# Kernel tuning notes

Hardware: AMD Instinct MI355X
Metric: run time of the kernel (lower is better)

The kernel has to match this reference:

```python
import jax, jax.numpy as jnp
import numpy as np

# ---- geometry constants (from init_kwargs options) ----
VIEWS, NDET, NX, NY = 360, 736, 512, 512
DVOX, DDET = 0.7, 1.2858
DSO, DOD = 595.0, 490.6
DSD = DSO + DOD
STEP = 0.0174533
END_ANGLE = STEP * VIEWS  # ~2*pi
EXTENT = 1


def _compute_indices():
    """CPU port of PixelIndexCal_cuda (fanflat mode, extent=1).
    Returns flat int64 indices of shape [NX*NY*VIEWS] (pixel-major, view inner)."""
    sVx, sVy = DVOX * NX, DVOX * NY
    alphas = np.linspace(0.0, END_ANGLE, VIEWS, endpoint=False)
    indX, indY = np.meshgrid(np.arange(NX, dtype=np.float64),
                             np.arange(NY, dtype=np.float64), indexing='ij')
    idx_all = np.empty((NX * NY, VIEWS), dtype=np.int64)
    for a in range(VIEWS):
        alpha = -alphas[a]
        c, s = np.cos(alpha), np.sin(alpha)
        P0x = -(sVx / 2 - DVOX / 2)
        P0y = sVy / 2 - DVOX / 2
        rot = lambda px, py: (px * c + py * s, -px * s + py * c)
        Px_, Py_ = rot(P0x, P0y)
        Pxx, Pxy = rot(P0x + DVOX, P0y)
        Pyx, Pyy = rot(P0x, P0y - DVOX)
        Py_, Pxy, Pyy = Py_ / DDET, Pxy / DDET, Pyy / DDET
        dXx, dXy = Pxx - Px_, Pxy - Py_
        dYx, dYy = Pyx - Px_, Pyy - Py_
        # per-pixel rotated coords
        Pix = Px_ + indX * dXx + indY * dYx
        Piy = Py_ + indX * dXy + indY * dYy
        # fanflat: source at (DSO, 0); ray hits detector plane at x = DSO-DSD
        vectX = Pix - DSO
        t = -DSD / vectX
        det = Piy * t + NDET / 2.0
        det = np.clip(det, 1.0, NDET - 2.0)
        idx_all[:, a] = (det + NDET * a).astype(np.int64).ravel()
    return idx_all.reshape(-1)


def _conv(x, w, b):
    y = jax.lax.conv_general_dilated(x, w, (1, 1), 'SAME',
                                     dimension_numbers=('NCHW', 'OIHW', 'NCHW'))
    return y + b[None, :, None, None]


def setup_inputs() -> dict:
    key = jax.random.key(0)
    ks = jax.random.split(key, 16)
    lin_std = 1.0 / np.sqrt(NDET)
    conv_std = 1.0 / np.sqrt(64 * 9)
    inp = {
        'x': jax.random.normal(ks[0], (1, 1, VIEWS, NDET), jnp.float32),
        'indices': jnp.asarray(_compute_indices()),
        'w1': jax.random.normal(ks[1], (NDET, NDET), jnp.float32) * lin_std,
        'b1': jnp.zeros((NDET,), jnp.float32),
        'w2': jax.random.normal(ks[2], (NDET, NDET), jnp.float32) * lin_std,
        'b2': jnp.zeros((NDET,), jnp.float32),
        'conv_in_w': jax.random.normal(ks[3], (64, 1, 3, 3), jnp.float32) * (1.0 / 3.0),
        'conv_in_b': jnp.zeros((64,), jnp.float32),
        'blk_w1': jax.random.normal(ks[4], (11, 64, 64, 3, 3), jnp.float32) * conv_std,
        'blk_b1': jnp.zeros((11, 64), jnp.float32),
        'blk_w2': jax.random.normal(ks[5], (11, 64, 64, 3, 3), jnp.float32) * conv_std,
        'blk_b2': jnp.zeros((11, 64), jnp.float32),
        'conv_out_w': jax.random.normal(ks[6], (1, 64, 3, 3), jnp.float32) * conv_std,
        'conv_out_b': jnp.zeros((1,), jnp.float32),
    }
    return inp


def reference(x, indices, w1, b1, w2, b2, conv_in_w, conv_in_b,
              blk_w1, blk_b1, blk_w2, blk_b2, conv_out_w, conv_out_b):
    # convf: two per-detector-row Linear+ReLU over last dim (nDetecU)
    h = jax.nn.relu(x @ w1.T + b1)
    h = jax.nn.relu(h @ w2.T + b2)
    # BackProjNet (learn=False): gather + sum over views, scale, flip
    sino = h.reshape(-1, 1, VIEWS * NDET)
    g = sino[:, :, indices]                         # [B,1,NX*NY*VIEWS]
    g = g.reshape(-1, 1, NX * NY, VIEWS * EXTENT)
    img = g.sum(axis=3) * ((END_ANGLE - 0.0) / (2 * VIEWS * EXTENT))
    img = img.reshape(-1, 1, NX, NY)
    img = jnp.flip(img, axis=(2, 3))
    # rCNN refinement: conv(1->64)+ReLU, 11 residual blocks, conv(64->1)
    y = jax.nn.relu(_conv(img, conv_in_w, conv_in_b))
    for i in range(11):
        z = _conv(y, blk_w1[i], blk_b1[i])
        z = jax.nn.relu(z)
        z = _conv(z, blk_w2[i], blk_b2[i])
        y = jax.nn.relu(y + z)
    out = _conv(y, conv_out_w, conv_out_b)
    return out
```

## Files before the change

### kernel.cpp

```cpp
#include <hip/hip_runtime.h>

#define VIEWS 360
#define NDET 736
#define NX 512
#define NY 512
#define NPIX (NX * NY)

typedef unsigned short u16;
typedef __attribute__((ext_vector_type(8))) short bf16x8;
typedef __attribute__((ext_vector_type(4))) float f32x4;

__device__ __forceinline__ u16 f2bf(float f) {
  unsigned u = __float_as_uint(f);
  return (u16)((u + 0x7fffu + ((u >> 16) & 1u)) >> 16);
}

__global__ __launch_bounds__(256) void linear_relu_kernel(
    const float* __restrict__ in, const float* __restrict__ w,
    const float* __restrict__ b, float* __restrict__ out) {
  __shared__ __align__(16) float xin[NDET];
  const int v = blockIdx.x;
  const float4* src4 = (const float4*)(in + v * NDET);
  float4* dst4 = (float4*)xin;
  for (int k = threadIdx.x; k < NDET / 4; k += 256) dst4[k] = src4[k];
  __syncthreads();

  for (int d = threadIdx.x; d < NDET; d += 256) {
    const float4* w4 = (const float4*)(w + d * NDET);
    float acc = 0.f;
#pragma unroll 8
    for (int k = 0; k < NDET / 4; ++k) {
      float4 xv = ((const float4*)xin)[k];
      float4 wv = w4[k];
      acc = fmaf(xv.x, wv.x, acc);
      acc = fmaf(xv.y, wv.y, acc);
      acc = fmaf(xv.z, wv.z, acc);
      acc = fmaf(xv.w, wv.w, acc);
    }
    out[v * NDET + d] = fmaxf(acc + b[d], 0.f);
  }
}

__global__ __launch_bounds__(256) void backproj_kernel(
    const float* __restrict__ sino, const int* __restrict__ idx,
    float* __restrict__ img) {
  __shared__ int lidx[256 * 77];
  const int t = threadIdx.x;
  const int p_base = blockIdx.x * 256;

  float a0 = 0.f, a1 = 0.f, a2 = 0.f, a3 = 0.f;

#pragma unroll 1
  for (int c = 0; c < 5; ++c) {
    if (c) __syncthreads();
#pragma unroll
    for (int k = 0; k < 18; ++k) {
      const int f = k * 256 + t;
      const int row = f / 18, col4 = f % 18;
      int4 v = *(const int4*)&idx[(size_t)(p_base + row) * VIEWS + c * 72 +
                                  col4 * 4];
      int* dst = &lidx[row * 77 + col4 * 4];
      dst[0] = v.x; dst[1] = v.y; dst[2] = v.z; dst[3] = v.w;
    }
    __syncthreads();
    const int* myrow = &lidx[t * 77];
#pragma unroll
    for (int j = 0; j < 72; j += 4) {
      a0 += sino[myrow[j + 0]];
      a1 += sino[myrow[j + 1]];
      a2 += sino[myrow[j + 2]];
      a3 += sino[myrow[j + 3]];
    }
  }

  const int p = p_base + t;
  const int ix = p >> 9, iy = p & 511;
  img[(NX - 1 - ix) * NY + (NY - 1 - iy)] =
      ((a0 + a1) + (a2 + a3)) * 0.00872665f;
}

__device__ __forceinline__ void load9(const float* __restrict__ base, int gx,
                                      int gy, float v[9]) {
  const bool xm = gx > 0, xp = gx < NX - 1, ym = gy > 0, yp = gy < NY - 1;
  const float* c = base + gy * NX + gx;
  v[0] = (ym && xm) ? c[-NX - 1] : 0.f;
  v[1] = (ym)       ? c[-NX]     : 0.f;
  v[2] = (ym && xp) ? c[-NX + 1] : 0.f;
  v[3] = (xm)       ? c[-1]      : 0.f;
  v[4] =               c[0];
  v[5] = (xp)       ? c[1]       : 0.f;
  v[6] = (yp && xm) ? c[NX - 1]  : 0.f;
  v[7] = (yp)       ? c[NX]      : 0.f;
  v[8] = (yp && xp) ? c[NX + 1]  : 0.f;
}

__device__ __forceinline__ float dot9(float a, const float v[9],
                                      const float* __restrict__ w) {
  a = fmaf(v[0], w[0], a);
  a = fmaf(v[1], w[1], a);
  a = fmaf(v[2], w[2], a);
  a = fmaf(v[3], w[3], a);
  a = fmaf(v[4], w[4], a);
  a = fmaf(v[5], w[5], a);
  a = fmaf(v[6], w[6], a);
  a = fmaf(v[7], w[7], a);
  a = fmaf(v[8], w[8], a);
  return a;
}

__global__ __launch_bounds__(256) void conv_in_kernel(
    const float* __restrict__ in, const float* __restrict__ w,
    const float* __restrict__ b, float* __restrict__ out) {
  const int p = blockIdx.x * 256 + threadIdx.x;
  const int gx = p & (NX - 1), gy = p >> 9;
  float v[9];
  load9(in, gx, gy, v);
  float4* o = (float4*)(out + (size_t)p * 64);
#pragma unroll
  for (int oq = 0; oq < 16; ++oq) {
    float4 r;
    r.x = fmaxf(dot9(b[oq * 4 + 0], v, w + (oq * 4 + 0) * 9), 0.f);
    r.y = fmaxf(dot9(b[oq * 4 + 1], v, w + (oq * 4 + 1) * 9), 0.f);
    r.z = fmaxf(dot9(b[oq * 4 + 2], v, w + (oq * 4 + 2) * 9), 0.f);
    r.w = fmaxf(dot9(b[oq * 4 + 3], v, w + (oq * 4 + 3) * 9), 0.f);
    o[oq] = r;
  }
}

__global__ __launch_bounds__(256) void prep_weights_kernel(
    const float* __restrict__ bw1, const float* __restrict__ bw2,
    u16* __restrict__ wR) {
  const int g = blockIdx.x * 256 + threadIdx.x;
  if (g >= 22 * 36864) return;
  const int li = g / 36864, r1 = g % 36864;
  const int s = r1 / 2048, r2 = r1 % 2048;
  const int lane = r2 / 32, r3 = r2 % 32;
  const int mf = r3 / 8, j = r3 % 8;
  const int tap = s >> 1, kb = s & 1;
  const int kg = lane >> 4, n = lane & 15;
  const int oc = mf * 16 + n;
  const int ic = kb * 32 + kg * 8 + j;
  const float* src = (li < 11) ? bw1 + li * 36864 : bw2 + (li - 11) * 36864;
  wR[g] = f2bf(src[(oc * 64 + ic) * 9 + tap]);
}

template <int IN_BF, int OUT_BF, int RELU, int ADDRES>
__global__ __launch_bounds__(256, 3) void conv64_mfma(
    const void* __restrict__ in_, const u16* __restrict__ wA,
    const float* __restrict__ bias, const float* __restrict__ res,
    void* __restrict__ out_) {
  __shared__ u16 lds[6 * 66 * 64];
  const int xb = (blockIdx.x & 7) * 64;
  const int yb = (int)(blockIdx.x >> 3) * 4;
  const int tid = threadIdx.x;

#pragma unroll 1
  for (int it = 0; it < 13; ++it) {
    const int g = it * 256 + tid;
    if (g < 3168) {
      const int icq = g & 7;
      const int xr = g >> 3;
      const int x66 = xr % 66;
      const int r = xr / 66;
      const int y = yb - 1 + r;
      const int x = xb - 1 + x66;
      uint4 d = {0u, 0u, 0u, 0u};
      if ((unsigned)y < 512u && (unsigned)x < 512u) {
        const size_t gi = ((size_t)((y << 9) + x)) * 64 + icq * 8;
        if (IN_BF) {
          d = *(const uint4*)&((const u16*)in_)[gi];
        } else {
          const float* s = &((const float*)in_)[gi];
          float4 f0 = *(const float4*)s;
          float4 f1 = *(const float4*)(s + 4);
          d.x = (unsigned)f2bf(f0.x) | ((unsigned)f2bf(f0.y) << 16);
          d.y = (unsigned)f2bf(f0.z) | ((unsigned)f2bf(f0.w) << 16);
          d.z = (unsigned)f2bf(f1.x) | ((unsigned)f2bf(f1.y) << 16);
          d.w = (unsigned)f2bf(f1.z) | ((unsigned)f2bf(f1.w) << 16);
        }
      }
      const int slot = icq ^ (x66 & 7);
      *(uint4*)&lds[(xr * 8 + slot) * 8] = d;
    }
  }
  __syncthreads();

  const int wv = tid >> 6;
  const int lane = tid & 63;
  const int n = lane & 15;
  const int kg = lane >> 4;

  f32x4 acc[4][4];
#pragma unroll
  for (int i = 0; i < 4; ++i)
#pragma unroll
    for (int j = 0; j < 4; ++j) acc[i][j] = (f32x4){0.f, 0.f, 0.f, 0.f};

  bf16x8 acur[4];
#pragma unroll
  for (int mf = 0; mf < 4; ++mf)
    acur[mf] = *(const bf16x8*)&wA[(size_t)lane * 32 + mf * 8];

#pragma unroll 1
  for (int s = 0; s < 18; ++s) {
    bf16x8 anxt[4];
    const int sn = (s < 17) ? s + 1 : s;
#pragma unroll
    for (int mf = 0; mf < 4; ++mf)
      anxt[mf] = *(const bf16x8*)&wA[((size_t)sn * 64 + lane) * 32 + mf * 8];

    const int tap = s >> 1, kb = s & 1;
    const int r = wv + tap / 3;
    const int dxp1 = tap % 3;
    const int q = kb * 4 + kg;

    bf16x8 bfr[4];
#pragma unroll
    for (int nf = 0; nf < 4; ++nf) {
      const int xi = dxp1 + nf * 16 + n;
      const int slot = q ^ (xi & 7);
      bfr[nf] = *(const bf16x8*)&lds[((r * 66 + xi) * 8 + slot) * 8];
    }
#pragma unroll
    for (int mf = 0; mf < 4; ++mf)
#pragma unroll
      for (int nf = 0; nf < 4; ++nf)
        acc[mf][nf] = __builtin_amdgcn_mfma_f32_16x16x32_bf16(
            acur[mf], bfr[nf], acc[mf][nf], 0, 0, 0);
#pragma unroll
    for (int mf = 0; mf < 4; ++mf) acur[mf] = anxt[mf];
  }

  const int y = yb + wv;
#pragma unroll
  for (int mf = 0; mf < 4; ++mf) {
    const float4 bv = *(const float4*)&bias[mf * 16 + kg * 4];
#pragma unroll
    for (int nf = 0; nf < 4; ++nf) {
      const int x = xb + nf * 16 + n;
      const size_t base = ((size_t)((y << 9) + x)) * 64 + mf * 16 + kg * 4;
      float v0 = acc[mf][nf][0] + bv.x;
      float v1 = acc[mf][nf][1] + bv.y;
      float v2 = acc[mf][nf][2] + bv.z;
      float v3 = acc[mf][nf][3] + bv.w;
      if (ADDRES) {
        float4 rr = *(const float4*)&res[base];
        v0 += rr.x; v1 += rr.y; v2 += rr.z; v3 += rr.w;
      }
      if (RELU) {
        v0 = fmaxf(v0, 0.f); v1 = fmaxf(v1, 0.f);
        v2 = fmaxf(v2, 0.f); v3 = fmaxf(v3, 0.f);
      }
      if (OUT_BF) {
        uint2 pk;
        pk.x = (unsigned)f2bf(v0) | ((unsigned)f2bf(v1) << 16);
        pk.y = (unsigned)f2bf(v2) | ((unsigned)f2bf(v3) << 16);
        *(uint2*)&((u16*)out_)[base] = pk;
      } else {
        *(float4*)&((float*)out_)[base] = (float4){v0, v1, v2, v3};
      }
    }
  }
}

__global__ __launch_bounds__(256) void conv_out_kernel(
    const float* __restrict__ in, const float* __restrict__ w,
    const float* __restrict__ b, float* __restrict__ out) {
  const int p = blockIdx.x * 256 + threadIdx.x;
  const int gx = p & (NX - 1), gy = p >> 9;
  float a = b[0];
#pragma unroll
  for (int ty = 0; ty < 3; ++ty) {
#pragma unroll
    for (int tx = 0; tx < 3; ++tx) {
      const int yy = gy + ty - 1, xx = gx + tx - 1;
      if ((unsigned)yy < 512u && (unsigned)xx < 512u) {
        const float4* q = (const float4*)(in + ((size_t)((yy << 9) + xx)) * 64);
        const int tap = ty * 3 + tx;
#pragma unroll
        for (int i = 0; i < 16; ++i) {
          float4 d = q[i];
          a = fmaf(d.x, w[(i * 4 + 0) * 9 + tap], a);
          a = fmaf(d.y, w[(i * 4 + 1) * 9 + tap], a);
          a = fmaf(d.z, w[(i * 4 + 2) * 9 + tap], a);
          a = fmaf(d.w, w[(i * 4 + 3) * 9 + tap], a);
        }
      }
    }
  }
  out[p] = a;
}

extern "C" void kernel_launch(void* const* d_in, const int* in_sizes, int n_in,
                              void* d_out, int out_size, void* d_ws,
                              size_t ws_size, hipStream_t stream) {
  const float* x      = (const float*)d_in[0];
  const int*   indices= (const int*)d_in[1];
  const float* w1     = (const float*)d_in[2];
  const float* b1     = (const float*)d_in[3];
  const float* w2     = (const float*)d_in[4];
  const float* b2     = (const float*)d_in[5];
  const float* cin_w  = (const float*)d_in[6];
  const float* cin_b  = (const float*)d_in[7];
  const float* bw1    = (const float*)d_in[8];
  const float* bb1    = (const float*)d_in[9];
  const float* bw2    = (const float*)d_in[10];
  const float* bb2    = (const float*)d_in[11];
  const float* cout_w = (const float*)d_in[12];
  const float* cout_b = (const float*)d_in[13];

  float* ws   = (float*)d_ws;
  float* h1   = ws;
  float* h2   = h1 + VIEWS * NDET;
  float* img  = h2 + VIEWS * NDET;
  float* yf   = img + NPIX;
  u16*  zb    = (u16*)(yf + 64 * NPIX);
  u16*  wAll  = zb + 64 * NPIX;

  prep_weights_kernel<<<(22 * 36864 + 255) / 256, 256, 0, stream>>>(bw1, bw2,
                                                                    wAll);
  linear_relu_kernel<<<VIEWS, 256, 0, stream>>>(x, w1, b1, h1);
  linear_relu_kernel<<<VIEWS, 256, 0, stream>>>(h1, w2, b2, h2);
  backproj_kernel<<<NPIX / 256, 256, 0, stream>>>(h2, indices, img);
  conv_in_kernel<<<NPIX / 256, 256, 0, stream>>>(img, cin_w, cin_b, yf);

  for (int i = 0; i < 11; ++i) {
    conv64_mfma<0, 1, 1, 0><<<1024, 256, 0, stream>>>(
        yf, wAll + i * 36864, bb1 + i * 64, nullptr, zb);
    conv64_mfma<1, 0, 1, 1><<<1024, 256, 0, stream>>>(
        zb, wAll + (11 + i) * 36864, bb2 + i * 64, yf, yf);
  }
  conv_out_kernel<<<NPIX / 256, 256, 0, stream>>>(yf, cout_w, cout_b,
                                                  (float*)d_out);
}
```

Before: 1.955 ms.

## Split conv64 input staging into two channel halves to halve LDS footprint

The 3x3 64-channel MFMA conv now stages its input halo tile in LDS in two 32-channel halves, looping over channel blocks outside the taps. This halves shared memory per block so occupancy can rise from 3 to 4 blocks per CU, and the weight layout is reordered to channel-block-major with a new XOR swizzle. In exchange it adds a second barrier and reload phase per block and drops explicit weight prefetch in favour of a partially unrolled tap loop.

```diff
diff --git a/kernel.cpp b/kernel.cpp
--- a/kernel.cpp
+++ b/kernel.cpp
@@ -136,7 +136,7 @@
   const int s = r1 / 2048, r2 = r1 % 2048;
   const int lane = r2 / 32, r3 = r2 % 32;
   const int mf = r3 / 8, j = r3 % 8;
-  const int tap = s >> 1, kb = s & 1;
+  const int kb = s / 9, tap = s % 9;
   const int kg = lane >> 4, n = lane & 15;
   const int oc = mf * 16 + n;
   const int ic = kb * 32 + kg * 8 + j;
@@ -145,46 +145,14 @@
 }
 
 template <int IN_BF, int OUT_BF, int RELU, int ADDRES>
-__global__ __launch_bounds__(256, 3) void conv64_mfma(
+__global__ __launch_bounds__(256, 4) void conv64_mfma(
     const void* __restrict__ in_, const u16* __restrict__ wA,
     const float* __restrict__ bias, const float* __restrict__ res,
     void* __restrict__ out_) {
-  __shared__ u16 lds[6 * 66 * 64];
+  __shared__ __align__(16) u16 lds[6 * 66 * 32];
   const int xb = (blockIdx.x & 7) * 64;
   const int yb = (int)(blockIdx.x >> 3) * 4;
   const int tid = threadIdx.x;
-
-#pragma unroll 1
-  for (int it = 0; it < 13; ++it) {
-    const int g = it * 256 + tid;
-    if (g < 3168) {
-      const int icq = g & 7;
-      const int xr = g >> 3;
-      const int x66 = xr % 66;
-      const int r = xr / 66;
-      const int y = yb - 1 + r;
-      const int x = xb - 1 + x66;
-      uint4 d = {0u, 0u, 0u, 0u};
-      if ((unsigned)y < 512u && (unsigned)x < 512u) {
-        const size_t gi = ((size_t)((y << 9) + x)) * 64 + icq * 8;
-        if (IN_BF) {
-          d = *(const uint4*)&((const u16*)in_)[gi];
-        } else {
-          const float* s = &((const float*)in_)[gi];
-          float4 f0 = *(const float4*)s;
-          float4 f1 = *(const float4*)(s + 4);
-          d.x = (unsigned)f2bf(f0.x) | ((unsigned)f2bf(f0.y) << 16);
-          d.y = (unsigned)f2bf(f0.z) | ((unsigned)f2bf(f0.w) << 16);
-          d.z = (unsigned)f2bf(f1.x) | ((unsigned)f2bf(f1.y) << 16);
-          d.w = (unsigned)f2bf(f1.z) | ((unsigned)f2bf(f1.w) << 16);
-        }
-      }
-      const int slot = icq ^ (x66 & 7);
-      *(uint4*)&lds[(xr * 8 + slot) * 8] = d;
-    }
-  }
-  __syncthreads();
-
   const int wv = tid >> 6;
   const int lane = tid & 63;
   const int n = lane & 15;
@@ -196,39 +164,66 @@
 #pragma unroll
     for (int j = 0; j < 4; ++j) acc[i][j] = (f32x4){0.f, 0.f, 0.f, 0.f};
 
-  bf16x8 acur[4];
-#pragma unroll
-  for (int mf = 0; mf < 4; ++mf)
-    acur[mf] = *(const bf16x8*)&wA[(size_t)lane * 32 + mf * 8];
-
 #pragma unroll 1
-  for (int s = 0; s < 18; ++s) {
-    bf16x8 anxt[4];
-    const int sn = (s < 17) ? s + 1 : s;
-#pragma unroll
-    for (int mf = 0; mf < 4; ++mf)
-      anxt[mf] = *(const bf16x8*)&wA[((size_t)sn * 64 + lane) * 32 + mf * 8];
-
-    const int tap = s >> 1, kb = s & 1;
-    const int r = wv + tap / 3;
-    const int dxp1 = tap % 3;
-    const int q = kb * 4 + kg;
-
-    bf16x8 bfr[4];
-#pragma unroll
-    for (int nf = 0; nf < 4; ++nf) {
-      const int xi = dxp1 + nf * 16 + n;
-      const int slot = q ^ (xi & 7);
-      bfr[nf] = *(const bf16x8*)&lds[((r * 66 + xi) * 8 + slot) * 8];
-    }
-#pragma unroll
-    for (int mf = 0; mf < 4; ++mf)
-#pragma unroll
-      for (int nf = 0; nf < 4; ++nf)
-        acc[mf][nf] = __builtin_amdgcn_mfma_f32_16x16x32_bf16(
-            acur[mf], bfr[nf], acc[mf][nf], 0, 0, 0);
-#pragma unroll
-    for (int mf = 0; mf < 4; ++mf) acur[mf] = anxt[mf];
+  for (int kb = 0; kb < 2; ++kb) {
+    if (kb) __syncthreads();
+#pragma unroll
+    for (int it = 0; it < 7; ++it) {
+      const int g = it * 256 + tid;
+      if (g < 1584) {
+        const int icq = g & 3;
+        const int xr = g >> 2;
+        const int x66 = xr % 66;
+        const int r = xr / 66;
+        const int y = yb - 1 + r;
+        const int x = xb - 1 + x66;
+        uint4 d = {0u, 0u, 0u, 0u};
+        if ((unsigned)y < 512u && (unsigned)x < 512u) {
+          const size_t gi =
+              ((size_t)((y << 9) + x)) * 64 + kb * 32 + icq * 8;
+          if (IN_BF) {
+            d = *(const uint4*)&((const u16*)in_)[gi];
+          } else {
+            const float* s = &((const float*)in_)[gi];
+            float4 f0 = *(const float4*)s;
+            float4 f1 = *(const float4*)(s + 4);
+            d.x = (unsigned)f2bf(f0.x) | ((unsigned)f2bf(f0.y) << 16);
+            d.y = (unsigned)f2bf(f0.z) | ((unsigned)f2bf(f0.w) << 16);
+            d.z = (unsigned)f2bf(f1.x) | ((unsigned)f2bf(f1.y) << 16);
+            d.w = (unsigned)f2bf(f1.z) | ((unsigned)f2bf(f1.w) << 16);
+          }
+        }
+        const int slot = icq ^ ((x66 >> 1) & 3);
+        *(uint4*)&lds[(xr * 4 + slot) * 8] = d;
+      }
+    }
+    __syncthreads();
+
+#pragma unroll 3
+    for (int tap = 0; tap < 9; ++tap) {
+      const int s = kb * 9 + tap;
+      bf16x8 av[4];
+#pragma unroll
+      for (int mf = 0; mf < 4; ++mf)
+        av[mf] = *(const bf16x8*)&wA[((size_t)s * 64 + lane) * 32 + mf * 8];
+
+      const int r = wv + tap / 3;
+      const int dxp1 = tap % 3;
+
+      bf16x8 bfr[4];
+#pragma unroll
+      for (int nf = 0; nf < 4; ++nf) {
+        const int xi = dxp1 + nf * 16 + n;
+        const int slot = kg ^ ((xi >> 1) & 3);
+        bfr[nf] = *(const bf16x8*)&lds[((r * 66 + xi) * 4 + slot) * 8];
+      }
+#pragma unroll
+      for (int mf = 0; mf < 4; ++mf)
+#pragma unroll
+        for (int nf = 0; nf < 4; ++nf)
+          acc[mf][nf] = __builtin_amdgcn_mfma_f32_16x16x32_bf16(
+              av[mf], bfr[nf], acc[mf][nf], 0, 0, 0);
+    }
   }
 
   const int y = yb + wv;
```

Result: faster. 1.835 ms (-6.2%).
